# Optimization experiments

Hardware: AMD Instinct MI355X
Metric: run time of the kernel (lower is better)

Reference implementation:

```python
import jax, jax.numpy as jnp
import numpy as np

NUM_HEADS = 16


def setup_inputs() -> dict:
    key = jax.random.key(0)
    ks = jax.random.split(key, 10)
    B, S, D = 2, 2048, 1024
    x = jax.random.normal(ks[0], (B, S, D), dtype=jnp.float32)
    mask = jax.random.randint(ks[1], (B, 1, 1, S), 0, 2, dtype=jnp.int32)
    scale = 1.0 / np.sqrt(D)
    wq = jax.random.normal(ks[2], (D, D), dtype=jnp.float32) * scale
    bq = jnp.zeros((D,), dtype=jnp.float32)
    wk = jax.random.normal(ks[3], (D, D), dtype=jnp.float32) * scale
    bk = jnp.zeros((D,), dtype=jnp.float32)
    wv = jax.random.normal(ks[4], (D, D), dtype=jnp.float32) * scale
    bv = jnp.zeros((D,), dtype=jnp.float32)
    wo = jax.random.normal(ks[5], (D, D), dtype=jnp.float32) * scale
    bo = jnp.zeros((D,), dtype=jnp.float32)
    return {"x": x, "mask": mask, "wq": wq, "bq": bq, "wk": wk, "bk": bk,
            "wv": wv, "bv": bv, "wo": wo, "bo": bo}


def reference(x, mask, wq, bq, wk, bk, wv, bv, wo, bo):
    B, S, D = x.shape
    H = NUM_HEADS
    dk = D // H

    def split_heads(t):
        # (B, S, D) -> (B, H, S, dk)
        return t.reshape(B, S, H, dk).transpose(0, 2, 1, 3)

    # PyTorch nn.Linear: y = x @ W^T + b
    q = split_heads(x @ wq.T + bq)
    k = split_heads(x @ wk.T + bk)
    v = split_heads(x @ wv.T + bv)

    # scaled dot-product attention with explicit score matrix (as original)
    logits = jnp.einsum('bhqd,bhkd->bhqk', q, k) / jnp.sqrt(jnp.float32(dk))
    logits = jnp.where(mask == 0, jnp.float32(-1e9), logits)
    attn_weights = jax.nn.softmax(logits, axis=-1)
    # dropout(p=0.1) is identity in eval mode (deterministic reference)
    attn = jnp.einsum('bhqk,bhkd->bhqd', attn_weights, v)

    attn = attn.transpose(0, 2, 1, 3).reshape(B, S, D)
    out = attn @ wo.T + bo
    return out, attn_weights
```

## Files before the change

### kernel.cpp

```cpp
#include <hip/hip_runtime.h>
#include <hip/hip_bf16.h>

#define DEV __device__ __forceinline__

typedef __attribute__((ext_vector_type(8))) __bf16 bf16x8;
typedef __attribute__((ext_vector_type(8))) short s16x8;
typedef __attribute__((ext_vector_type(4))) float f32x4;
typedef __attribute__((ext_vector_type(2))) unsigned long long u64x2;

DEV f32x4 mfma16(s16x8 a, s16x8 b, f32x4 c){
  return __builtin_amdgcn_mfma_f32_16x16x32_bf16(
      __builtin_bit_cast(bf16x8, a), __builtin_bit_cast(bf16x8, b), c, 0, 0, 0);
}

DEV unsigned int cvtpk(float a, float b){
  float2 t; t.x = a; t.y = b;
  __hip_bfloat162 h = __float22bfloat162_rn(t);
  unsigned int r;
  __builtin_memcpy(&r, &h, 4);
  return r;
}

DEV unsigned short f2bf(float f){
  __hip_bfloat16 h = __float2bfloat16(f);
  unsigned short r;
  __builtin_memcpy(&r, &h, 2);
  return r;
}

DEV float bf2f(unsigned short u){
  return __builtin_bit_cast(float, ((unsigned int)u) << 16);
}

DEV unsigned long long pack4(float4 v){
  return (unsigned long long)cvtpk(v.x, v.y) | ((unsigned long long)cvtpk(v.z, v.w) << 32);
}

DEV unsigned long long pack4f(float a, float b, float c, float d){
  return (unsigned long long)cvtpk(a, b) | ((unsigned long long)cvtpk(c, d) << 32);
}

DEV void async16(const void* g, void* l){
  __builtin_amdgcn_global_load_lds(
      (const __attribute__((address_space(1))) unsigned int*)g,
      (__attribute__((address_space(3))) unsigned int*)l, 16, 0, 0);
}

__global__ __launch_bounds__(256) void cvt_kernel(
    const float* __restrict__ x, const float* __restrict__ wq, const float* __restrict__ wk,
    const float* __restrict__ wv, const float* __restrict__ wo,
    const float* __restrict__ bq, const float* __restrict__ bk, const float* __restrict__ bv,
    unsigned long long* __restrict__ xb, unsigned long long* __restrict__ wqkvb,
    unsigned long long* __restrict__ wob, float4* __restrict__ bqkv)
{
  const int i = blockIdx.x * 256 + threadIdx.x;
  const int X4 = 1048576, W4 = 262144;
  if (i < X4){
    xb[i] = pack4(((const float4*)x)[i]);
  } else if (i < X4 + 3*W4){
    int j = i - X4;
    const float* src = (j < W4) ? wq : (j < 2*W4) ? wk : wv;
    int jj = (j < W4) ? j : (j < 2*W4) ? (j - W4) : (j - 2*W4);
    wqkvb[j] = pack4(((const float4*)src)[jj]);
  } else if (i < X4 + 4*W4){
    int j = i - X4 - 3*W4;
    wob[j] = pack4(((const float4*)wo)[j]);
  } else if (i < X4 + 4*W4 + 768){
    int j = i - X4 - 4*W4;
    const float* src = (j < 256) ? bq : (j < 512) ? bk : bv;
    int jj = (j < 256) ? j : (j < 512) ? (j - 256) : (j - 512);
    bqkv[j] = ((const float4*)src)[jj];
  }
}

__global__ __launch_bounds__(256) void gemm_qkv(
    const unsigned short* __restrict__ A,
    const unsigned short* __restrict__ B,
    const float* __restrict__ bias,
    unsigned short* __restrict__ oq,
    unsigned short* __restrict__ okk,
    unsigned short* __restrict__ ovt)
{
  __shared__ __align__(16) char smem[32768];
  char* As = smem;
  char* Bs = smem + 16384;
  const int tid = threadIdx.x;
  const int l = tid & 63, w = tid >> 6, g = l >> 4;

  const int orig = blockIdx.x;
  const int lin = (orig & 7) * 96 + (orig >> 3);
  const int m0 = (lin / 24) * 128, n0 = (lin % 24) * 128;
  const int rowbytes = 2048;

  f32x4 acc[4][4] = {};
  const int wr = w >> 1, wc = w & 1;
  const int wm = wr * 64, wn = wc * 64;

  const int srow = w * 32 + (l >> 3);
  const int scol = (((l & 7) ^ (l >> 3)) << 4);
  const char* Abp = (const char*)A + (size_t)(m0 + srow) * rowbytes + scol;
  const char* Bbp = (const char*)B + (size_t)(n0 + srow) * rowbytes + scol;
  char* Asw = As + w * 4096;
  char* Bsw = Bs + w * 4096;

  int aoff[4][2], boff[4][2];
  for (int mf = 0; mf < 4; ++mf)
    for (int ks = 0; ks < 2; ++ks){
      int ra = wm + mf * 16 + (l & 15);
      aoff[mf][ks] = ra * 128 + ((ks * 64 + g * 16) ^ ((l & 7) << 4));
      int rb = wn + mf * 16 + (l & 15);
      boff[mf][ks] = rb * 128 + ((ks * 64 + g * 16) ^ ((l & 7) << 4));
    }

  for (int kt = 0; kt < 16; ++kt){
    const char* ab = Abp + kt * 128;
    const char* bb = Bbp + kt * 128;
    for (int i = 0; i < 4; ++i){
      async16(ab + (size_t)i * 8 * rowbytes, Asw + i * 1024);
      async16(bb + (size_t)i * 8 * rowbytes, Bsw + i * 1024);
    }
    __syncthreads();
    for (int ks = 0; ks < 2; ++ks){
      s16x8 af[4], bf[4];
      for (int mf = 0; mf < 4; ++mf) af[mf] = *(const s16x8*)(As + aoff[mf][ks]);
      for (int nf = 0; nf < 4; ++nf) bf[nf] = *(const s16x8*)(Bs + boff[nf][ks]);
      for (int mf = 0; mf < 4; ++mf)
        for (int nf = 0; nf < 4; ++nf)
          acc[mf][nf] = mfma16(af[mf], bf[nf], acc[mf][nf]);
    }
    __syncthreads();
  }

  if (n0 >= 2048){
    for (int nf = 0; nf < 4; ++nf){
      int nloc = wn + nf * 16 + (l & 15);
      float bs = bias[n0 + nloc];
      for (int mf = 0; mf < 4; ++mf){
        int mby = (wm + mf * 16 + g * 4) * 2;
        unsigned long long pk = pack4f(acc[mf][nf][0] + bs, acc[mf][nf][1] + bs,
                                       acc[mf][nf][2] + bs, acc[mf][nf][3] + bs);
        *(unsigned long long*)(smem + nloc * 256 + (mby ^ ((nloc & 15) << 4))) = pk;
      }
    }
    __syncthreads();
    int b2 = m0 >> 11, s0 = m0 & 2047;
    for (int i = 0; i < 8; ++i){
      int idx = i * 256 + tid;
      int row = idx >> 4, c8 = (idx & 15) * 8;
      s16x8 vv = *(const s16x8*)(smem + row * 256 + ((c8 * 2) ^ ((row & 15) << 4)));
      *(s16x8*)(ovt + (size_t)(b2 * 1024 + (n0 - 2048) + row) * 2048 + s0 + c8) = vv;
    }
    return;
  }

  for (int mf = 0; mf < 4; ++mf)
    for (int nf = 0; nf < 4; ++nf)
      for (int r = 0; r < 4; ++r){
        int grow = m0 + wm + mf * 16 + g * 4 + r;
        int n = n0 + wn + nf * 16 + (l & 15);
        float v = acc[mf][nf][r] + bias[n];
        if (n < 1024) oq [(size_t)grow * 1024 + n]          = f2bf(v);
        else          okk[(size_t)grow * 1024 + (n - 1024)] = f2bf(v);
      }
}

__global__ __launch_bounds__(256) void gemm_out(
    const unsigned short* __restrict__ A,
    const unsigned short* __restrict__ B,
    const float* __restrict__ bias,
    float* __restrict__ of)
{
  __shared__ __align__(16) char smem[32768];
  char* As = smem;
  char* Bs = smem + 16384;
  const int tid = threadIdx.x, l = tid & 63, w = tid >> 6, g = l >> 4;
  const int orig = blockIdx.x;
  const int lin = (orig & 7) * 64 + (orig >> 3);
  const int m0 = (lin >> 4) * 128, n0 = (lin & 15) * 64;
  const int rowbytes = 2048;

  f32x4 acc[2][4] = {};
  const int wm = w * 32;

  const int scol = (((l & 7) ^ (l >> 3)) << 4);
  const char* Abp = (const char*)A + (size_t)(m0 + w * 32 + (l >> 3)) * rowbytes + scol;
  const char* Bbp = (const char*)B + (size_t)(n0 + w * 16 + (l >> 3)) * rowbytes + scol;
  char* Asw = As + w * 4096;
  char* Bsw = Bs + w * 2048;

  int aoff[2][2], boff[4][2];
  for (int ks = 0; ks < 2; ++ks){
    for (int mf = 0; mf < 2; ++mf){
      int ra = wm + mf * 16 + (l & 15);
      aoff[mf][ks] = ra * 128 + ((ks * 64 + g * 16) ^ ((l & 7) << 4));
    }
    for (int nf = 0; nf < 4; ++nf){
      int rb = nf * 16 + (l & 15);
      boff[nf][ks] = rb * 128 + ((ks * 64 + g * 16) ^ ((l & 7) << 4));
    }
  }

  for (int kt = 0; kt < 16; ++kt){
    for (int i = 0; i < 4; ++i)
      async16(Abp + kt * 128 + (size_t)i * 8 * rowbytes, Asw + i * 1024);
    for (int i = 0; i < 2; ++i)
      async16(Bbp + kt * 128 + (size_t)i * 8 * rowbytes, Bsw + i * 1024);
    __syncthreads();
    for (int ks = 0; ks < 2; ++ks){
      s16x8 af[2], bf[4];
      for (int mf = 0; mf < 2; ++mf) af[mf] = *(const s16x8*)(As + aoff[mf][ks]);
      for (int nf = 0; nf < 4; ++nf) bf[nf] = *(const s16x8*)(Bs + boff[nf][ks]);
      for (int mf = 0; mf < 2; ++mf)
        for (int nf = 0; nf < 4; ++nf)
          acc[mf][nf] = mfma16(af[mf], bf[nf], acc[mf][nf]);
    }
    __syncthreads();
  }

  __syncthreads();
  char* stg = smem + w * 8192;
  float bv4[4];
  for (int nf = 0; nf < 4; ++nf) bv4[nf] = bias[n0 + nf * 16 + (l & 15)];
  for (int mf = 0; mf < 2; ++mf)
    for (int nf = 0; nf < 4; ++nf)
      for (int r = 0; r < 4; ++r){
        int row = mf * 16 + g * 4 + r;
        int colb = (nf * 16 + (l & 15)) * 4;
        *(float*)(stg + row * 256 + (colb ^ ((row & 7) << 4))) = acc[mf][nf][r] + bv4[nf];
      }
  __syncthreads();
  for (int t = 0; t < 8; ++t){
    int row = t * 4 + (l >> 4);
    int colb = ((l & 15) * 16) ^ ((row & 7) << 4);
    f32x4 v = *(const f32x4*)(stg + row * 256 + colb);
    __builtin_nontemporal_store(v, (f32x4*)&of[(size_t)(m0 + wm + row) * 1024 + n0 + (l & 15) * 4]);
  }
}

__global__ __launch_bounds__(256, 3) void attn_kernel(
    const unsigned short* __restrict__ qb,
    const unsigned short* __restrict__ kb,
    const unsigned short* __restrict__ vtb,
    const int* __restrict__ mask,
    float* __restrict__ Pout,
    unsigned short* __restrict__ attnb)
{
  const int flat = blockIdx.x;
  const int sw = (flat & 7) * 256 + (flat >> 3);
  const int qt = sw & 63, h = (sw >> 6) & 15, b = sw >> 10;
  const int tid = threadIdx.x, l = tid & 63, w = tid >> 6, g = l >> 4;
  const int q0 = qt * 32;

  __shared__ float maskadd[2048];
  __shared__ float zpart[4][32];
  __shared__ __align__(16) unsigned long long estu[2048];
  __shared__ __align__(16) float comb[2048];

  for (int i = tid; i < 2048; i += 256)
    maskadd[i] = mask[b * 2048 + i] ? 0.0f : -1e30f;

  s16x8 qf[2][2];
  for (int mf = 0; mf < 2; ++mf)
    for (int ks = 0; ks < 2; ++ks)
      qf[mf][ks] = *(const s16x8*)(qb + (size_t)(b*2048 + q0 + mf*16 + (l&15)) * 1024
                                   + h*64 + ks*32 + g*8);

  const unsigned short* Kb = kb + (size_t)b * 2048 * 1024 + h * 64;
  const unsigned short* Vb = vtb + ((size_t)b * 1024 + h * 64) * 2048;

  __syncthreads();

  float zacc[2] = {0.0f, 0.0f};
  for (int j = 0; j < 8; ++j){
    int kk0 = j * 256 + w * 64;
    f32x4 c[2][4] = {};
    for (int nh = 0; nh < 2; ++nh){
      s16x8 kf[2][2];
      for (int n2 = 0; n2 < 2; ++n2)
        for (int ks = 0; ks < 2; ++ks)
          kf[n2][ks] = *(const s16x8*)(Kb + (size_t)(kk0 + (nh*2+n2)*16 + (l&15)) * 1024 + ks*32 + g*8);
      __builtin_amdgcn_s_setprio(1);
      for (int ks = 0; ks < 2; ++ks)
        for (int mf = 0; mf < 2; ++mf)
          for (int n2 = 0; n2 < 2; ++n2)
            c[mf][nh*2+n2] = mfma16(kf[n2][ks], qf[mf][ks], c[mf][nh*2+n2]);
      __builtin_amdgcn_s_setprio(0);
    }
    for (int nf = 0; nf < 4; ++nf){
      f32x4 ma = *(const f32x4*)&maskadd[kk0 + nf*16 + g*4];
      for (int mf = 0; mf < 2; ++mf)
        for (int r = 0; r < 4; ++r)
          zacc[mf] += __expf(fmaf(c[mf][nf][r], 0.125f, ma[r]));
    }
  }
  for (int mf = 0; mf < 2; ++mf){
    float z = zacc[mf];
    z += __shfl_xor(z, 16, 64);
    z += __shfl_xor(z, 32, 64);
    zacc[mf] = z;
  }
  if (g == 0){
    zpart[w][l & 15]        = zacc[0];
    zpart[w][16 + (l & 15)] = zacc[1];
  }
  __syncthreads();
  float zinv[2];
  for (int mf = 0; mf < 2; ++mf){
    int row = mf*16 + (l & 15);
    zinv[mf] = 1.0f / (zpart[0][row] + zpart[1][row] + zpart[2][row] + zpart[3][row]);
  }

  float* Pb = Pout + ((size_t)(b*16 + h) * 2048 + q0) * 2048;
  f32x4 pv[2][4] = {};
  char* estw = (char*)estu + w * 4096;
  for (int j = 0; j < 8; ++j){
    int kk0 = j * 256 + w * 64;
    f32x4 c[2][4] = {};
    for (int nh = 0; nh < 2; ++nh){
      s16x8 kf[2][2];
      for (int n2 = 0; n2 < 2; ++n2)
        for (int ks = 0; ks < 2; ++ks)
          kf[n2][ks] = *(const s16x8*)(Kb + (size_t)(kk0 + (nh*2+n2)*16 + (l&15)) * 1024 + ks*32 + g*8);
      __builtin_amdgcn_s_setprio(1);
      for (int ks = 0; ks < 2; ++ks)
        for (int mf = 0; mf < 2; ++mf)
          for (int n2 = 0; n2 < 2; ++n2)
            c[mf][nh*2+n2] = mfma16(kf[n2][ks], qf[mf][ks], c[mf][nh*2+n2]);
      __builtin_amdgcn_s_setprio(0);
    }
    for (int mf = 0; mf < 2; ++mf){
      int q = mf*16 + (l & 15);
      for (int nf = 0; nf < 4; ++nf){
        f32x4 ma = *(const f32x4*)&maskadd[kk0 + nf*16 + g*4];
        f32x4 p4;
        for (int r = 0; r < 4; ++r)
          p4[r] = __expf(fmaf(c[mf][nf][r], 0.125f, ma[r])) * zinv[mf];
        *(unsigned long long*)(estw + q*128 + ((nf*32 + g*8) ^ ((q & 7) << 4))) =
            pack4f(p4[0], p4[1], p4[2], p4[3]);
      }
    }
    s16x8 pa[2][2];
    for (int mf = 0; mf < 2; ++mf)
      for (int ks = 0; ks < 2; ++ks){
        int q = mf*16 + (l & 15);
        const unsigned long long* pp =
            (const unsigned long long*)(estw + q*128 + ((ks*64 + g*16) ^ ((q & 7) << 4)));
        u64x2 t; t[0] = pp[0]; t[1] = pp[1];
        pa[mf][ks] = __builtin_bit_cast(s16x8, t);
      }
    for (int dh = 0; dh < 2; ++dh){
      s16x8 vf[2][2];
      for (int d2 = 0; d2 < 2; ++d2)
        for (int ks = 0; ks < 2; ++ks)
          vf[d2][ks] = *(const s16x8*)(Vb + (size_t)((dh*2+d2)*16 + (l&15)) * 2048 + kk0 + ks*32 + g*8);
      __builtin_amdgcn_s_setprio(1);
      for (int ks = 0; ks < 2; ++ks)
        for (int mf = 0; mf < 2; ++mf)
          for (int d2 = 0; d2 < 2; ++d2)
            pv[mf][dh*2+d2] = mfma16(pa[mf][ks], vf[d2][ks], pv[mf][dh*2+d2]);
      __builtin_amdgcn_s_setprio(0);
    }
    for (int t = 0; t < 8; ++t){
      int row = t * 4 + (l >> 4);
      unsigned long long pk =
          *(const unsigned long long*)(estw + row*128 + (((l & 15) * 8) ^ ((row & 7) << 4)));
      f32x4 ps;
      ps[0] = bf2f((unsigned short)(pk      ));
      ps[1] = bf2f((unsigned short)(pk >> 16));
      ps[2] = bf2f((unsigned short)(pk >> 32));
      ps[3] = bf2f((unsigned short)(pk >> 48));
      __builtin_nontemporal_store(ps, (f32x4*)&Pb[(size_t)row * 2048 + kk0 + (l & 15) * 4]);
    }
  }

  __syncthreads();
  char* est = (char*)estu;
  char* bufw = (w == 0) ? (char*)maskadd : (w == 1) ? est : (w == 2) ? (est + 8192) : (char*)comb;
  for (int mf = 0; mf < 2; ++mf)
    for (int dn = 0; dn < 4; ++dn)
      for (int r = 0; r < 4; ++r){
        int row = mf*16 + g*4 + r, col = dn*16 + (l & 15);
        *(float*)(bufw + row*256 + ((col*4) ^ (((row >> 2) & 3) << 6))) = pv[mf][dn][r];
      }
  __syncthreads();
  {
    int row = tid >> 3, c8 = (tid & 7) * 8;
    int off = row*256 + ((c8*4) ^ (((row >> 2) & 3) << 6));
    f32x4 s0_ = *(f32x4*)((char*)maskadd + off);
    f32x4 s1_ = *(f32x4*)((char*)maskadd + off + 16);
    s0_ += *(f32x4*)(est + off);          s1_ += *(f32x4*)(est + off + 16);
    s0_ += *(f32x4*)(est + 8192 + off);   s1_ += *(f32x4*)(est + 8192 + off + 16);
    s0_ += *(f32x4*)((char*)comb + off);  s1_ += *(f32x4*)((char*)comb + off + 16);
    u64x2 ov;
    ov[0] = pack4f(s0_[0], s0_[1], s0_[2], s0_[3]);
    ov[1] = pack4f(s1_[0], s1_[1], s1_[2], s1_[3]);
    *(u64x2*)&attnb[(size_t)(b*2048 + q0 + row) * 1024 + h*64 + c8] = ov;
  }
}

extern "C" void kernel_launch(void* const* d_in, const int* in_sizes, int n_in,
                              void* d_out, int out_size, void* d_ws, size_t ws_size,
                              hipStream_t stream)
{
  const float* x  = (const float*)d_in[0];
  const int* mask = (const int*)d_in[1];
  const float* wq = (const float*)d_in[2];
  const float* bq = (const float*)d_in[3];
  const float* wk = (const float*)d_in[4];
  const float* bk = (const float*)d_in[5];
  const float* wv = (const float*)d_in[6];
  const float* bv = (const float*)d_in[7];
  const float* wo = (const float*)d_in[8];
  const float* bo = (const float*)d_in[9];

  char* ws = (char*)d_ws;
  unsigned short* xb    = (unsigned short*)(ws);
  unsigned short* wqkvb = (unsigned short*)(ws + 8388608);
  unsigned short* wob   = (unsigned short*)(ws + 14680064);
  float*          bqkv  = (float*)(ws + 16777216);
  unsigned short* qb    = (unsigned short*)(ws + 16793600);
  unsigned short* kb    = (unsigned short*)(ws + 25182208);
  unsigned short* vtb   = (unsigned short*)(ws + 33570816);
  unsigned short* attnb = (unsigned short*)(ws + 41959424);

  float* fout = (float*)d_out;
  float* Pout = fout + 4194304;

  cvt_kernel<<<8195, 256, 0, stream>>>(x, wq, wk, wv, wo, bq, bk, bv,
                                       (unsigned long long*)xb, (unsigned long long*)wqkvb,
                                       (unsigned long long*)wob, (float4*)bqkv);
  gemm_qkv<<<768, 256, 0, stream>>>(xb, wqkvb, bqkv, qb, kb, vtb);
  attn_kernel<<<2048, 256, 0, stream>>>(qb, kb, vtb, mask, Pout, attnb);
  gemm_out<<<512, 256, 0, stream>>>(attnb, wob, bo, fout);
}
```

Baseline: 266.0 us.

## Split softmax normalizer pass into separate kernel and raise attention occupancy

The first pass that computes per-row softmax denominators moves into its own zcalc kernel, which writes inverse sums to workspace. The attention kernel then only runs the probability/PV pass, with launch bounds raised to 4 blocks per CU, and each wave now takes a contiguous 512-key range. The P store is also moved ahead of the PV MFMAs so stores can overlap with compute. The cost is an extra launch and a second read of Q, K and mask, traded for lower register/LDS pressure and higher occupancy.

```diff
diff --git a/kernel.cpp b/kernel.cpp
--- a/kernel.cpp
+++ b/kernel.cpp
@@ -237,13 +237,11 @@
   }
 }
 
-__global__ __launch_bounds__(256, 3) void attn_kernel(
+__global__ __launch_bounds__(256) void zcalc_kernel(
     const unsigned short* __restrict__ qb,
     const unsigned short* __restrict__ kb,
-    const unsigned short* __restrict__ vtb,
     const int* __restrict__ mask,
-    float* __restrict__ Pout,
-    unsigned short* __restrict__ attnb)
+    float* __restrict__ zinvg)
 {
   const int flat = blockIdx.x;
   const int sw = (flat & 7) * 256 + (flat >> 3);
@@ -253,8 +251,6 @@
 
   __shared__ float maskadd[2048];
   __shared__ float zpart[4][32];
-  __shared__ __align__(16) unsigned long long estu[2048];
-  __shared__ __align__(16) float comb[2048];
 
   for (int i = tid; i < 2048; i += 256)
     maskadd[i] = mask[b * 2048 + i] ? 0.0f : -1e30f;
@@ -266,13 +262,11 @@
                                    + h*64 + ks*32 + g*8);
 
   const unsigned short* Kb = kb + (size_t)b * 2048 * 1024 + h * 64;
-  const unsigned short* Vb = vtb + ((size_t)b * 1024 + h * 64) * 2048;
-
   __syncthreads();
 
   float zacc[2] = {0.0f, 0.0f};
-  for (int j = 0; j < 8; ++j){
-    int kk0 = j * 256 + w * 64;
+  for (int jj = 0; jj < 8; ++jj){
+    const int kk0 = w * 512 + jj * 64;
     f32x4 c[2][4] = {};
     for (int nh = 0; nh < 2; ++nh){
       s16x8 kf[2][2];
@@ -304,17 +298,55 @@
     zpart[w][16 + (l & 15)] = zacc[1];
   }
   __syncthreads();
-  float zinv[2];
-  for (int mf = 0; mf < 2; ++mf){
-    int row = mf*16 + (l & 15);
-    zinv[mf] = 1.0f / (zpart[0][row] + zpart[1][row] + zpart[2][row] + zpart[3][row]);
-  }
+  if (tid < 32){
+    float s = zpart[0][tid] + zpart[1][tid] + zpart[2][tid] + zpart[3][tid];
+    zinvg[(size_t)(b*16 + h) * 2048 + q0 + tid] = 1.0f / s;
+  }
+}
+
+__global__ __launch_bounds__(256, 4) void attn_kernel(
+    const unsigned short* __restrict__ qb,
+    const unsigned short* __restrict__ kb,
+    const unsigned short* __restrict__ vtb,
+    const int* __restrict__ mask,
+    const float* __restrict__ zinvg,
+    float* __restrict__ Pout,
+    unsigned short* __restrict__ attnb)
+{
+  const int flat = blockIdx.x;
+  const int sw = (flat & 7) * 256 + (flat >> 3);
+  const int qt = sw & 63, h = (sw >> 6) & 15, b = sw >> 10;
+  const int tid = threadIdx.x, l = tid & 63, w = tid >> 6, g = l >> 4;
+  const int q0 = qt * 32;
+
+  __shared__ __align__(16) unsigned long long estu[2048];
+  __shared__ float maskadd[2048];
+  __shared__ __align__(16) float comb[2048];
+  __shared__ float zfull[32];
+
+  for (int i = tid; i < 2048; i += 256)
+    maskadd[i] = mask[b * 2048 + i] ? 0.0f : -1e30f;
+  if (tid < 32)
+    zfull[tid] = zinvg[(size_t)(b*16 + h) * 2048 + q0 + tid];
+
+  s16x8 qf[2][2];
+  for (int mf = 0; mf < 2; ++mf)
+    for (int ks = 0; ks < 2; ++ks)
+      qf[mf][ks] = *(const s16x8*)(qb + (size_t)(b*2048 + q0 + mf*16 + (l&15)) * 1024
+                                   + h*64 + ks*32 + g*8);
+
+  const unsigned short* Kb = kb + (size_t)b * 2048 * 1024 + h * 64;
+  const unsigned short* Vb = vtb + ((size_t)b * 1024 + h * 64) * 2048;
+
+  __syncthreads();
+  float zinv[2] = { zfull[l & 15], zfull[16 + (l & 15)] };
 
   float* Pb = Pout + ((size_t)(b*16 + h) * 2048 + q0) * 2048;
   f32x4 pv[2][4] = {};
   char* estw = (char*)estu + w * 4096;
-  for (int j = 0; j < 8; ++j){
-    int kk0 = j * 256 + w * 64;
+
+  for (int jj = 0; jj < 8; ++jj){
+    const int kk0 = w * 512 + jj * 64;
     f32x4 c[2][4] = {};
     for (int nh = 0; nh < 2; ++nh){
       s16x8 kf[2][2];
@@ -345,9 +377,20 @@
         int q = mf*16 + (l & 15);
         const unsigned long long* pp =
             (const unsigned long long*)(estw + q*128 + ((ks*64 + g*16) ^ ((q & 7) << 4)));
-        u64x2 t; t[0] = pp[0]; t[1] = pp[1];
-        pa[mf][ks] = __builtin_bit_cast(s16x8, t);
-      }
+        u64x2 t2; t2[0] = pp[0]; t2[1] = pp[1];
+        pa[mf][ks] = __builtin_bit_cast(s16x8, t2);
+      }
+    for (int t = 0; t < 8; ++t){
+      int row = t * 4 + (l >> 4);
+      unsigned long long pk =
+          *(const unsigned long long*)(estw + row*128 + (((l & 15) * 8) ^ ((row & 7) << 4)));
+      f32x4 ps;
+      ps[0] = bf2f((unsigned short)(pk      ));
+      ps[1] = bf2f((unsigned short)(pk >> 16));
+      ps[2] = bf2f((unsigned short)(pk >> 32));
+      ps[3] = bf2f((unsigned short)(pk >> 48));
+      __builtin_nontemporal_store(ps, (f32x4*)&Pb[(size_t)row * 2048 + kk0 + (l & 15) * 4]);
+    }
     for (int dh = 0; dh < 2; ++dh){
       s16x8 vf[2][2];
       for (int d2 = 0; d2 < 2; ++d2)
@@ -360,22 +403,12 @@
             pv[mf][dh*2+d2] = mfma16(pa[mf][ks], vf[d2][ks], pv[mf][dh*2+d2]);
       __builtin_amdgcn_s_setprio(0);
     }
-    for (int t = 0; t < 8; ++t){
-      int row = t * 4 + (l >> 4);
-      unsigned long long pk =
-          *(const unsigned long long*)(estw + row*128 + (((l & 15) * 8) ^ ((row & 7) << 4)));
-      f32x4 ps;
-      ps[0] = bf2f((unsigned short)(pk      ));
-      ps[1] = bf2f((unsigned short)(pk >> 16));
-      ps[2] = bf2f((unsigned short)(pk >> 32));
-      ps[3] = bf2f((unsigned short)(pk >> 48));
-      __builtin_nontemporal_store(ps, (f32x4*)&Pb[(size_t)row * 2048 + kk0 + (l & 15) * 4]);
-    }
-  }
-
-  __syncthreads();
-  char* est = (char*)estu;
-  char* bufw = (w == 0) ? (char*)maskadd : (w == 1) ? est : (w == 2) ? (est + 8192) : (char*)comb;
+  }
+
+  __syncthreads();
+  char* bufw = (w == 0) ? (char*)estu
+             : (w == 1) ? ((char*)estu + 8192)
+             : (w == 2) ? (char*)maskadd : (char*)comb;
   for (int mf = 0; mf < 2; ++mf)
     for (int dn = 0; dn < 4; ++dn)
       for (int r = 0; r < 4; ++r){
@@ -386,11 +419,11 @@
   {
     int row = tid >> 3, c8 = (tid & 7) * 8;
     int off = row*256 + ((c8*4) ^ (((row >> 2) & 3) << 6));
-    f32x4 s0_ = *(f32x4*)((char*)maskadd + off);
-    f32x4 s1_ = *(f32x4*)((char*)maskadd + off + 16);
-    s0_ += *(f32x4*)(est + off);          s1_ += *(f32x4*)(est + off + 16);
-    s0_ += *(f32x4*)(est + 8192 + off);   s1_ += *(f32x4*)(est + 8192 + off + 16);
-    s0_ += *(f32x4*)((char*)comb + off);  s1_ += *(f32x4*)((char*)comb + off + 16);
+    f32x4 s0_ = *(f32x4*)((char*)estu + off);
+    f32x4 s1_ = *(f32x4*)((char*)estu + off + 16);
+    s0_ += *(f32x4*)((char*)estu + 8192 + off);  s1_ += *(f32x4*)((char*)estu + 8192 + off + 16);
+    s0_ += *(f32x4*)((char*)maskadd + off);      s1_ += *(f32x4*)((char*)maskadd + off + 16);
+    s0_ += *(f32x4*)((char*)comb + off);         s1_ += *(f32x4*)((char*)comb + off + 16);
     u64x2 ov;
     ov[0] = pack4f(s0_[0], s0_[1], s0_[2], s0_[3]);
     ov[1] = pack4f(s1_[0], s1_[1], s1_[2], s1_[3]);
@@ -422,6 +455,7 @@
   unsigned short* kb    = (unsigned short*)(ws + 25182208);
   unsigned short* vtb   = (unsigned short*)(ws + 33570816);
   unsigned short* attnb = (unsigned short*)(ws + 41959424);
+  float*          zinvg = (float*)(ws + 50348032);
 
   float* fout = (float*)d_out;
   float* Pout = fout + 4194304;
@@ -430,6 +464,7 @@
                                        (unsigned long long*)xb, (unsigned long long*)wqkvb,
                                        (unsigned long long*)wob, (float4*)bqkv);
   gemm_qkv<<<768, 256, 0, stream>>>(xb, wqkvb, bqkv, qb, kb, vtb);
-  attn_kernel<<<2048, 256, 0, stream>>>(qb, kb, vtb, mask, Pout, attnb);
+  zcalc_kernel<<<2048, 256, 0, stream>>>(qb, kb, mask, zinvg);
+  attn_kernel<<<2048, 256, 0, stream>>>(qb, kb, vtb, mask, zinvg, Pout, attnb);
   gemm_out<<<512, 256, 0, stream>>>(attnb, wob, bo, fout);
 }
```

Result: slower. 283.3 us (+6.5%).
